# Kernel optimization log

Hardware: AMD Instinct MI355X
Metric: run time of the kernel (lower is better)

Reference implementation:

```python
import jax, jax.numpy as jnp
import numpy as np

ALPHA = 0.98
DELTA = 2.0
R = 0.5
EPS = 1e-6


def setup_inputs() -> dict:
    key = jax.random.key(0)
    x = jax.random.uniform(key, (32, 128, 4000), dtype=jnp.float32)
    return {"x": x}


def reference(x):
    # smooth[t] = (1-alpha)*x[t] + alpha*smooth[t-1], smooth[0] = x[0]
    # Expressed as an affine recurrence s_t = A_t * s_{t-1} + B_t and solved
    # with a log-depth associative scan (Blelchoch-style) over the time axis.
    alpha = jnp.asarray(ALPHA, dtype=x.dtype)
    # A: multiplier per step; A[...,0]=0 so s_0 = B_0 = x[...,0]
    A = jnp.full_like(x, alpha).at[..., 0].set(0.0)
    B = jnp.concatenate([x[..., :1], (1.0 - alpha) * x[..., 1:]], axis=-1)

    def combine(c1, c2):
        a1, b1 = c1
        a2, b2 = c2
        return (a2 * a1, a2 * b1 + b2)

    _, smooth = jax.lax.associative_scan(combine, (A, B), axis=-1)

    pcen = (x / (smooth + EPS) ** ALPHA + DELTA) ** R - DELTA ** R
    return pcen
```

## Files before the change

### kernel.cpp

```cpp
#include <hip/hip_runtime.h>
#include <math.h>

#define T_LEN   4000
#define CHUNK   256
#define NCHUNK  16

__device__ __forceinline__ float pcen_elem(float xv, float s) {
    const float ALPHA = 0.98f;
    const float DELTA = 2.0f;
    const float SQRT_DELTA = 1.4142135623730951f;
    const float EPS = 1e-6f;
    float p = exp2f(-ALPHA * log2f(s + EPS));
    return sqrtf(fmaf(xv, p, DELTA)) - SQRT_DELTA;
}

__global__ __launch_bounds__(256, 4) void pcen_kernel(const float* __restrict__ x,
                                                      float* __restrict__ out,
                                                      int nrows) {
    const float ALPHA = 0.98f;
    const float OMA   = 0.02f;
    const float A4    = 0.92236816f;

    const int lane = threadIdx.x & 63;
    const int wave = threadIdx.x >> 6;
    const int row  = blockIdx.x * 4 + wave;
    if (row >= nrows) return;

    const float* __restrict__ xr   = x   + (size_t)row * T_LEN;
    float* __restrict__       orow = out + (size_t)row * T_LEN;

    float s_prev = 0.0f;

#pragma unroll
    for (int c = 0; c < NCHUNK; ++c) {
        const int t0 = c * CHUNK + lane * 4;
        const bool valid = (t0 < T_LEN);

        float4 v = make_float4(0.f, 0.f, 0.f, 0.f);
        if (valid) v = *reinterpret_cast<const float4*>(xr + t0);

        float a, b;
        if (!valid) {
            a = 1.0f; b = 0.0f;
        } else if (t0 == 0) {
            a = 0.0f;
            b = v.x;
            b = fmaf(ALPHA, b, OMA * v.y);
            b = fmaf(ALPHA, b, OMA * v.z);
            b = fmaf(ALPHA, b, OMA * v.w);
        } else {
            a = A4;
            b = OMA * v.x;
            b = fmaf(ALPHA, b, OMA * v.y);
            b = fmaf(ALPHA, b, OMA * v.z);
            b = fmaf(ALPHA, b, OMA * v.w);
        }

        float ai = a, bi = b;
#pragma unroll
        for (int d = 1; d < 64; d <<= 1) {
            const float au = __shfl_up(ai, d);
            const float bu = __shfl_up(bi, d);
            if (lane >= d) {
                bi = fmaf(ai, bu, bi);
                ai = ai * au;
            }
        }

        float ae = __shfl_up(ai, 1);
        float be = __shfl_up(bi, 1);
        if (lane == 0) { ae = 1.0f; be = 0.0f; }
        float s = fmaf(ae, s_prev, be);

        const float a63 = __shfl(ai, 63);
        const float b63 = __shfl(bi, 63);
        const float s_next = fmaf(a63, s_prev, b63);

        if (valid) {
            float4 o;
            if (t0 == 0) {
                s = v.x;
            } else {
                s = fmaf(ALPHA, s, OMA * v.x);
            }
            o.x = pcen_elem(v.x, s);
            s = fmaf(ALPHA, s, OMA * v.y);
            o.y = pcen_elem(v.y, s);
            s = fmaf(ALPHA, s, OMA * v.z);
            o.z = pcen_elem(v.z, s);
            s = fmaf(ALPHA, s, OMA * v.w);
            o.w = pcen_elem(v.w, s);
            *reinterpret_cast<float4*>(orow + t0) = o;
        }

        s_prev = s_next;
    }
}

extern "C" void kernel_launch(void* const* d_in, const int* in_sizes, int n_in,
                              void* d_out, int out_size, void* d_ws, size_t ws_size,
                              hipStream_t stream) {
    const float* x = (const float*)d_in[0];
    float* out = (float*)d_out;
    const int nrows = in_sizes[0] / T_LEN;
    const int rows_per_block = 4;
    const int grid = (nrows + rows_per_block - 1) / rows_per_block;
    pcen_kernel<<<grid, 256, 0, stream>>>(x, out, nrows);
}
```

Measured before the change: 112.9 us.

## Use constant decay powers in wave scan, preload row, nontemporal stores

Replaces the two-component affine wave scan with a scan only on the additive term, since the multipliers are known powers of alpha and can be precomputed per lane. This halves the shuffles per step and removes the predicated multiply. All 16 chunk loads for the row are issued up front to hide memory latency. Output uses nontemporal stores to avoid cache pollution. The costs are higher register pressure from holding 64 floats per lane, and relying on hardcoded power constants.

```diff
diff --git a/kernel.cpp b/kernel.cpp
--- a/kernel.cpp
+++ b/kernel.cpp
@@ -4,6 +4,8 @@
 #define T_LEN   4000
 #define CHUNK   256
 #define NCHUNK  16
+
+typedef float v4f __attribute__((ext_vector_type(4)));
 
 __device__ __forceinline__ float pcen_elem(float xv, float s) {
     const float ALPHA = 0.98f;
@@ -19,7 +21,13 @@
                                                       int nrows) {
     const float ALPHA = 0.98f;
     const float OMA   = 0.02f;
-    const float A4    = 0.92236816f;
+    const float R1   = 0.92236816f;
+    const float R2   = 0.85076302f;
+    const float R4   = 0.72379771f;
+    const float R8   = 0.52388312f;
+    const float R16  = 0.27445352f;
+    const float R32  = 0.07532473f;
+    const float A256 = 0.00567381f;
 
     const int lane = threadIdx.x & 63;
     const int wave = threadIdx.x >> 6;
@@ -29,71 +37,63 @@
     const float* __restrict__ xr   = x   + (size_t)row * T_LEN;
     float* __restrict__       orow = out + (size_t)row * T_LEN;
 
+    float4 v[NCHUNK];
+#pragma unroll
+    for (int c = 0; c < NCHUNK; ++c) {
+        const int t0 = c * CHUNK + lane * 4;
+        if (t0 < T_LEN) v[c] = *reinterpret_cast<const float4*>(xr + t0);
+        else            v[c] = make_float4(0.f, 0.f, 0.f, 0.f);
+    }
+
+    float powl = 1.0f;
+    powl *= (lane & 1)  ? R1  : 1.0f;
+    powl *= (lane & 2)  ? R2  : 1.0f;
+    powl *= (lane & 4)  ? R4  : 1.0f;
+    powl *= (lane & 8)  ? R8  : 1.0f;
+    powl *= (lane & 16) ? R16 : 1.0f;
+    powl *= (lane & 32) ? R32 : 1.0f;
+
     float s_prev = 0.0f;
-
 #pragma unroll
     for (int c = 0; c < NCHUNK; ++c) {
         const int t0 = c * CHUNK + lane * 4;
         const bool valid = (t0 < T_LEN);
+        const float4 vc = v[c];
 
-        float4 v = make_float4(0.f, 0.f, 0.f, 0.f);
-        if (valid) v = *reinterpret_cast<const float4*>(xr + t0);
+        float b = (t0 == 0) ? vc.x : OMA * vc.x;
+        b = fmaf(ALPHA, b, OMA * vc.y);
+        b = fmaf(ALPHA, b, OMA * vc.z);
+        b = fmaf(ALPHA, b, OMA * vc.w);
 
-        float a, b;
-        if (!valid) {
-            a = 1.0f; b = 0.0f;
-        } else if (t0 == 0) {
-            a = 0.0f;
-            b = v.x;
-            b = fmaf(ALPHA, b, OMA * v.y);
-            b = fmaf(ALPHA, b, OMA * v.z);
-            b = fmaf(ALPHA, b, OMA * v.w);
-        } else {
-            a = A4;
-            b = OMA * v.x;
-            b = fmaf(ALPHA, b, OMA * v.y);
-            b = fmaf(ALPHA, b, OMA * v.z);
-            b = fmaf(ALPHA, b, OMA * v.w);
-        }
+        float bi = b;
+        { float bu = __shfl_up(bi, 1);  bi = fmaf(lane >= 1  ? R1  : 0.f, bu, bi); }
+        { float bu = __shfl_up(bi, 2);  bi = fmaf(lane >= 2  ? R2  : 0.f, bu, bi); }
+        { float bu = __shfl_up(bi, 4);  bi = fmaf(lane >= 4  ? R4  : 0.f, bu, bi); }
+        { float bu = __shfl_up(bi, 8);  bi = fmaf(lane >= 8  ? R8  : 0.f, bu, bi); }
+        { float bu = __shfl_up(bi, 16); bi = fmaf(lane >= 16 ? R16 : 0.f, bu, bi); }
+        { float bu = __shfl_up(bi, 32); bi = fmaf(lane >= 32 ? R32 : 0.f, bu, bi); }
 
-        float ai = a, bi = b;
-#pragma unroll
-        for (int d = 1; d < 64; d <<= 1) {
-            const float au = __shfl_up(ai, d);
-            const float bu = __shfl_up(bi, d);
-            if (lane >= d) {
-                bi = fmaf(ai, bu, bi);
-                ai = ai * au;
-            }
-        }
+        float be = __shfl_up(bi, 1);
+        if (lane == 0) be = 0.0f;
+        float s = fmaf(powl, s_prev, be);
 
-        float ae = __shfl_up(ai, 1);
-        float be = __shfl_up(bi, 1);
-        if (lane == 0) { ae = 1.0f; be = 0.0f; }
-        float s = fmaf(ae, s_prev, be);
-
-        const float a63 = __shfl(ai, 63);
         const float b63 = __shfl(bi, 63);
-        const float s_next = fmaf(a63, s_prev, b63);
+        s_prev = fmaf(A256, s_prev, b63);
 
         if (valid) {
             float4 o;
-            if (t0 == 0) {
-                s = v.x;
-            } else {
-                s = fmaf(ALPHA, s, OMA * v.x);
-            }
-            o.x = pcen_elem(v.x, s);
-            s = fmaf(ALPHA, s, OMA * v.y);
-            o.y = pcen_elem(v.y, s);
-            s = fmaf(ALPHA, s, OMA * v.z);
-            o.z = pcen_elem(v.z, s);
-            s = fmaf(ALPHA, s, OMA * v.w);
-            o.w = pcen_elem(v.w, s);
-            *reinterpret_cast<float4*>(orow + t0) = o;
+            if (t0 == 0) s = vc.x;
+            else         s = fmaf(ALPHA, s, OMA * vc.x);
+            o.x = pcen_elem(vc.x, s);
+            s = fmaf(ALPHA, s, OMA * vc.y);
+            o.y = pcen_elem(vc.y, s);
+            s = fmaf(ALPHA, s, OMA * vc.z);
+            o.z = pcen_elem(vc.z, s);
+            s = fmaf(ALPHA, s, OMA * vc.w);
+            o.w = pcen_elem(vc.w, s);
+            v4f ov = { o.x, o.y, o.z, o.w };
+            __builtin_nontemporal_store(ov, reinterpret_cast<v4f*>(orow + t0));
         }
-
-        s_prev = s_next;
     }
 }
 
```

Result: no change. 114.9 us (+1.8%).
